# Kernel tuning notes

Measured on AMD Instinct MI355X. Metric: run time of the kernel, lower is better.

The kernel has to match this reference:

```python
import jax, jax.numpy as jnp
import numpy as np

IMG = 800          # original image H = W
OUT = 7            # pooled output size
SR = 2             # sampling_ratio
CANON_S = 224.0    # canonical_scale
CANON_L = 4.0      # canonical_level
EPS = 1e-6
KMIN, KMAX = 2, 5  # -log2 of first/last scale


def _bilinear_gather(feat, b_idx, y, x):
    """feat: [B,C,H,W]; b_idx: [N] int; y,x: [N,S] float sample coords.
    Returns [N,S,C]. Faithful to torchvision roi_align bilinear_interpolate
    (aligned=False semantics)."""
    B, C, H, W = feat.shape
    valid = (y > -1.0) & (y < H) & (x > -1.0) & (x < W)
    y = jnp.clip(y, 0.0, None)
    x = jnp.clip(x, 0.0, None)
    yl = jnp.minimum(jnp.floor(y).astype(jnp.int32), H - 1)
    xl = jnp.minimum(jnp.floor(x).astype(jnp.int32), W - 1)
    yh = jnp.minimum(yl + 1, H - 1)
    xh = jnp.minimum(xl + 1, W - 1)
    y = jnp.where(yl >= H - 1, yl.astype(y.dtype), y)
    x = jnp.where(xl >= W - 1, xl.astype(x.dtype), x)
    ly = y - yl
    lx = x - xl
    hy = 1.0 - ly
    hx = 1.0 - lx
    flat = feat.transpose(0, 2, 3, 1).reshape(B * H * W, C)  # [B*H*W, C]
    base = b_idx[:, None] * (H * W)                            # [N,1]

    def g(yy, xx):
        return flat[base + yy * W + xx]  # gather -> [N,S,C]

    val = ((hy * hx)[..., None] * g(yl, xl)
           + (hy * lx)[..., None] * g(yl, xh)
           + (ly * hx)[..., None] * g(yh, xl)
           + (ly * lx)[..., None] * g(yh, xh))
    return jnp.where(valid[..., None], val, 0.0)


def _roi_align(feat, rois, scale):
    """Single-level RoIAlign, aligned=False. rois: [N,5] = (batch_idx,x1,y1,x2,y2)."""
    N = rois.shape[0]
    C = feat.shape[1]
    b_idx = rois[:, 0].astype(jnp.int32)
    x1 = rois[:, 1] * scale
    y1 = rois[:, 2] * scale
    x2 = rois[:, 3] * scale
    y2 = rois[:, 4] * scale
    roi_w = jnp.maximum(x2 - x1, 1.0)
    roi_h = jnp.maximum(y2 - y1, 1.0)
    bin_w = roi_w / OUT
    bin_h = roi_h / OUT
    # sample offsets within the roi, in units of bins: [OUT*SR]
    off = (jnp.arange(OUT, dtype=feat.dtype)[:, None]
           + (jnp.arange(SR, dtype=feat.dtype)[None, :] + 0.5) / SR).reshape(-1)
    ys = y1[:, None] + off[None, :] * bin_h[:, None]  # [N, OUT*SR]
    xs = x1[:, None] + off[None, :] * bin_w[:, None]  # [N, OUT*SR]
    S = OUT * SR
    Y = jnp.broadcast_to(ys[:, :, None], (N, S, S)).reshape(N, S * S)
    X = jnp.broadcast_to(xs[:, None, :], (N, S, S)).reshape(N, S * S)
    val = _bilinear_gather(feat, b_idx, Y, X)          # [N, S*S, C]
    val = val.reshape(N, OUT, SR, OUT, SR, C).mean(axis=(2, 4))  # avg over samples
    return val.transpose(0, 3, 1, 2)                   # [N, C, OUT, OUT]


def setup_inputs() -> dict:
    key = jax.random.key(0)
    ks = jax.random.split(key, 7)
    feats = {}
    for i, hw in enumerate([200, 100, 50, 25]):
        feats[f"feat{i}"] = jax.random.normal(ks[i], (2, 256, hw, hw), dtype=jnp.float32)
    # boxes [2, 256, 4] in (x1,y1,x2,y2), sizes log-uniform in [16, ~590] px
    xy1 = jax.random.uniform(ks[4], (2, 256, 2), minval=0.0, maxval=IMG - 32.0)
    sz = 2.0 ** jax.random.uniform(ks[5], (2, 256, 2), minval=4.0, maxval=9.2)
    xy2 = jnp.minimum(xy1 + sz, float(IMG))
    boxes = jnp.concatenate([xy1, xy2], axis=-1).astype(jnp.float32)
    return {**feats, "boxes": boxes}


def reference(feat0, feat1, feat2, feat3, boxes):
    feats = [feat0, feat1, feat2, feat3]
    # _infer_scale: round(log2(feat_size / image_size)) -> power-of-two scale
    scales = [2.0 ** round(float(np.log2(f.shape[2] / IMG))) for f in feats]
    # _convert_to_roi_format
    B, Nb, _ = boxes.shape
    ids = jnp.repeat(jnp.arange(B, dtype=boxes.dtype), Nb)[:, None]
    rois = jnp.concatenate([ids, boxes.reshape(B * Nb, 4)], axis=1)  # [N,5]
    # LevelMapper (FPN eq.1)
    s = jnp.sqrt((rois[:, 3] - rois[:, 1]) * (rois[:, 4] - rois[:, 2]))
    lvls = jnp.floor(CANON_L + jnp.log2(s / CANON_S) + EPS)
    lvls = jnp.clip(lvls, KMIN, KMAX).astype(jnp.int32) - KMIN  # [N] in {0..3}
    out = jnp.zeros((B * Nb, feat0.shape[1], OUT, OUT), dtype=feat0.dtype)
    for lvl, (f, sc) in enumerate(zip(feats, scales)):
        r = _roi_align(f, rois, sc)
        out = jnp.where((lvls == lvl)[:, None, None, None], r, out)
    return out
```

## Files before the change

### kernel.cpp

```cpp
#include <hip/hip_runtime.h>
#include <hip/hip_bf16.h>


#define IMGC   256
#define OUTP   7
#define NBIN   49
#define SAMP   14
#define BT     128
#define TILE_LD (BT + 1)

#define WS_O1 20480000
#define WS_O2 25600000
#define WS_O3 26880000
#define WS_TOT 27200000

__global__ __launch_bounds__(256) void transpose_cl_kernel(
    const float* __restrict__ f0, const float* __restrict__ f1,
    const float* __restrict__ f2, const float* __restrict__ f3,
    float* __restrict__ ws)
{
    __shared__ float t[64][65];

    int bx = blockIdx.x;
    int lvl, r;
    if (bx < 5000)      { lvl = 0; r = bx; }
    else if (bx < 6256) { lvl = 1; r = bx - 5000; }
    else if (bx < 6576) { lvl = 2; r = bx - 6256; }
    else                { lvl = 3; r = bx - 6576; }

    const int  Mtab[4]  = {40000, 10000, 2500, 625};
    const int  Mttab[4] = {625, 157, 40, 10};
    const int  wsoff[4] = {0, WS_O1, WS_O2, WS_O3};

    const float* in = (lvl == 0) ? f0 : (lvl == 1) ? f1 : (lvl == 2) ? f2 : f3;
    float* outp = ws + wsoff[lvl];
    int M = Mtab[lvl];
    int Mt = Mttab[lvl];

    int mt   = r % Mt;
    int rest = r / Mt;
    int ct   = rest & 3;
    int bb   = rest >> 2;

    int tx = threadIdx.x & 63;
    int tg = threadIdx.x >> 6;
    int m0 = mt * 64;

    {
        int m = m0 + tx;
        if (m < M) {
            int base = (bb * IMGC + ct * 64) * M + m;
            #pragma unroll
            for (int k = 0; k < 16; ++k) {
                int cc = tg * 16 + k;
                t[cc][tx] = in[base + cc * M];
            }
        }
    }
    __syncthreads();
    #pragma unroll
    for (int k = 0; k < 16; ++k) {
        int mm = tg * 16 + k;
        int m = m0 + mm;
        if (m < M)
            outp[(bb * M + m) * IMGC + ct * 64 + tx] = t[tx][mm];
    }
}

template <bool CL>
__global__ __launch_bounds__(BT) void roialign_kernel(
    const float* __restrict__ f0, const float* __restrict__ f1,
    const float* __restrict__ f2, const float* __restrict__ f3,
    const float* __restrict__ boxes, float* __restrict__ out)
{
    __shared__ float s_ly[SAMP], s_wy[SAMP], s_lx[SAMP], s_wx[SAMP];
    __shared__ int   s_yol[SAMP], s_yoh[SAMP], s_xol[SAMP], s_xoh[SAMP];
    __shared__ float tile[NBIN * TILE_LD];

    const int tid = threadIdx.x;
    const int blk = blockIdx.x;
    const int n   = blk >> 1;
    const int c0  = (blk & 1) * BT;
    const int b   = n >> 8;

    const float x1 = boxes[n * 4 + 0];
    const float y1 = boxes[n * 4 + 1];
    const float x2 = boxes[n * 4 + 2];
    const float y2 = boxes[n * 4 + 3];

    float s = sqrtf(fmaxf((x2 - x1) * (y2 - y1), 1e-12f));
    float lf = floorf(4.0f + log2f(s / 224.0f) + 1e-6f);
    int lvl = (int)fminf(fmaxf(lf, 2.0f), 5.0f) - 2;

    const int   Htab[4]  = {200, 100, 50, 25};
    const float sctab[4] = {0.25f, 0.125f, 0.0625f, 0.03125f};
    const int   H = Htab[lvl];
    const int   W = H;
    const float scale = sctab[lvl];
    const float* fp = (lvl == 0) ? f0 : (lvl == 1) ? f1 : (lvl == 2) ? f2 : f3;

    const float x1s = x1 * scale, y1s = y1 * scale;
    const float x2s = x2 * scale, y2s = y2 * scale;
    const float roi_w = fmaxf(x2s - x1s, 1.0f);
    const float roi_h = fmaxf(y2s - y1s, 1.0f);
    const float bin_w = roi_w * (1.0f / OUTP);
    const float bin_h = roi_h * (1.0f / OUTP);

    if (tid < SAMP) {
        int t = tid;
        float off = (float)(t >> 1) + 0.25f + 0.5f * (float)(t & 1);
        float y = y1s + off * bin_h;
        float v = (y > -1.0f && y < (float)H) ? 1.0f : 0.0f;
        y = fmaxf(y, 0.0f);
        int yl = min((int)y, H - 1);
        int yh = min(yl + 1, H - 1);
        if (yl >= H - 1) y = (float)yl;
        s_ly[t] = y - (float)yl;
        s_wy[t] = v;
        if (CL) { s_yol[t] = ((b * H + yl) * W) * IMGC; s_yoh[t] = ((b * H + yh) * W) * IMGC; }
        else    { s_yol[t] = yl * W;                    s_yoh[t] = yh * W; }
    } else if (tid >= 64 && tid < 64 + SAMP) {
        int t = tid - 64;
        float off = (float)(t >> 1) + 0.25f + 0.5f * (float)(t & 1);
        float x = x1s + off * bin_w;
        float v = (x > -1.0f && x < (float)W) ? 1.0f : 0.0f;
        x = fmaxf(x, 0.0f);
        int xl = min((int)x, W - 1);
        int xh = min(xl + 1, W - 1);
        if (xl >= W - 1) x = (float)xl;
        s_lx[t] = x - (float)xl;
        s_wx[t] = v;
        if (CL) { s_xol[t] = xl * IMGC; s_xoh[t] = xh * IMGC; }
        else    { s_xol[t] = xl;        s_xoh[t] = xh; }
    }
    __syncthreads();

    const int c = c0 + tid;
    const int tb = CL ? c : (b * IMGC + c) * (H * W);

    for (int bin = 0; bin < NBIN; ++bin) {
        int ph = bin / OUTP;
        int pw = bin - ph * OUTP;
        float acc = 0.0f;
        #pragma unroll
        for (int sy = 0; sy < 2; ++sy) {
            #pragma unroll
            for (int sx = 0; sx < 2; ++sx) {
                int i = 2 * ph + sy;
                int j = 2 * pw + sx;
                float ly = s_ly[i], lx = s_lx[j];
                float hy = 1.0f - ly, hx = 1.0f - lx;
                float wm = s_wy[i] * s_wx[j];
                int yol = s_yol[i], yoh = s_yoh[i];
                int xol = s_xol[j], xoh = s_xoh[j];
                float v1 = fp[tb + yol + xol];
                float v2 = fp[tb + yol + xoh];
                float v3 = fp[tb + yoh + xol];
                float v4 = fp[tb + yoh + xoh];
                acc += wm * (hy * (hx * v1 + lx * v2) + ly * (hx * v3 + lx * v4));
            }
        }
        tile[bin * TILE_LD + tid] = acc * 0.25f;
    }
    __syncthreads();

    const int outbase = n * (IMGC * NBIN) + c0 * NBIN;
    for (int t = tid; t < BT * NBIN; t += BT) {
        int cl = t / NBIN;
        int bb = t - cl * NBIN;
        out[outbase + t] = tile[bb * TILE_LD + cl];
    }
}

extern "C" void kernel_launch(void* const* d_in, const int* in_sizes, int n_in,
                              void* d_out, int out_size, void* d_ws, size_t ws_size,
                              hipStream_t stream) {
    const float* f0    = (const float*)d_in[0];
    const float* f1    = (const float*)d_in[1];
    const float* f2    = (const float*)d_in[2];
    const float* f3    = (const float*)d_in[3];
    const float* boxes = (const float*)d_in[4];
    float* out = (float*)d_out;

    const bool use_cl = ws_size >= (size_t)WS_TOT * sizeof(float);

    if (use_cl) {
        float* w = (float*)d_ws;
        transpose_cl_kernel<<<6656, 256, 0, stream>>>(f0, f1, f2, f3, w);
        roialign_kernel<true><<<1024, BT, 0, stream>>>(
            w, w + WS_O1, w + WS_O2, w + WS_O3, boxes, out);
    } else {
        roialign_kernel<false><<<1024, BT, 0, stream>>>(f0, f1, f2, f3, boxes, out);
    }
}
```

Baseline: 202.2 us.

## Vectorize transpose and channels-last RoIAlign with float4 loads and precomputed weights

The transpose kernel gains a float4 path for full tiles, reading four spatial elements and writing four channels per thread through a padded shared tile. The channels-last RoIAlign kernel now has each thread handle four channels with float4 gathers, with work spread across bins by thread groups. It also precomputes the combined bilinear weights for all 14x14 sample pairs in shared memory. This cuts the number of memory instructions in the bandwidth-bound transpose and gather, at the cost of extra shared memory and a possible drop in occupancy.

```diff
diff --git a/kernel.cpp b/kernel.cpp
--- a/kernel.cpp
+++ b/kernel.cpp
@@ -7,7 +7,8 @@
 #define NBIN   49
 #define SAMP   14
 #define BT     128
-#define TILE_LD (BT + 1)
+#define TLD    132
+#define SLD    68
 
 #define WS_O1 20480000
 #define WS_O2 25600000
@@ -19,7 +20,7 @@
     const float* __restrict__ f2, const float* __restrict__ f3,
     float* __restrict__ ws)
 {
-    __shared__ float t[64][65];
+    __shared__ float t[64 * SLD];
 
     int bx = blockIdx.x;
     int lvl, r;
@@ -34,48 +35,75 @@
 
     const float* in = (lvl == 0) ? f0 : (lvl == 1) ? f1 : (lvl == 2) ? f2 : f3;
     float* outp = ws + wsoff[lvl];
-    int M = Mtab[lvl];
-    int Mt = Mttab[lvl];
+    const int M  = Mtab[lvl];
+    const int Mt = Mttab[lvl];
 
     int mt   = r % Mt;
     int rest = r / Mt;
     int ct   = rest & 3;
     int bb   = rest >> 2;
-
-    int tx = threadIdx.x & 63;
-    int tg = threadIdx.x >> 6;
-    int m0 = mt * 64;
-
-    {
-        int m = m0 + tx;
-        if (m < M) {
-            int base = (bb * IMGC + ct * 64) * M + m;
-            #pragma unroll
-            for (int k = 0; k < 16; ++k) {
-                int cc = tg * 16 + k;
-                t[cc][tx] = in[base + cc * M];
+    int m0   = mt * 64;
+
+    const bool vec = (m0 + 64 <= M) && ((M & 3) == 0);
+
+    if (vec) {
+        int mq = threadIdx.x & 15;
+        int cg = threadIdx.x >> 4;
+        const float* ibase = in + (bb * IMGC + ct * 64) * M + m0;
+        #pragma unroll
+        for (int j = 0; j < 4; ++j) {
+            int c = cg + 16 * j;
+            float4 v = *(const float4*)(ibase + c * M + 4 * mq);
+            *(float4*)&t[c * SLD + 4 * mq] = v;
+        }
+        __syncthreads();
+        int cq = threadIdx.x & 15;
+        int mr = threadIdx.x >> 4;
+        float* obase = outp + (bb * M + m0) * IMGC + ct * 64;
+        #pragma unroll
+        for (int j = 0; j < 4; ++j) {
+            int m = mr + 16 * j;
+            float4 v;
+            v.x = t[(4 * cq + 0) * SLD + m];
+            v.y = t[(4 * cq + 1) * SLD + m];
+            v.z = t[(4 * cq + 2) * SLD + m];
+            v.w = t[(4 * cq + 3) * SLD + m];
+            *(float4*)(obase + m * IMGC + 4 * cq) = v;
+        }
+    } else {
+        int tx = threadIdx.x & 63;
+        int tg = threadIdx.x >> 6;
+        {
+            int m = m0 + tx;
+            if (m < M) {
+                int base = (bb * IMGC + ct * 64) * M + m;
+                #pragma unroll
+                for (int k = 0; k < 16; ++k) {
+                    int cc = tg * 16 + k;
+                    t[cc * SLD + tx] = in[base + cc * M];
+                }
             }
         }
-    }
-    __syncthreads();
-    #pragma unroll
-    for (int k = 0; k < 16; ++k) {
-        int mm = tg * 16 + k;
-        int m = m0 + mm;
-        if (m < M)
-            outp[(bb * M + m) * IMGC + ct * 64 + tx] = t[tx][mm];
+        __syncthreads();
+        #pragma unroll
+        for (int k = 0; k < 16; ++k) {
+            int mm = tg * 16 + k;
+            int m = m0 + mm;
+            if (m < M)
+                outp[(bb * M + m) * IMGC + ct * 64 + tx] = t[tx * SLD + mm];
+        }
     }
 }
 
-template <bool CL>
-__global__ __launch_bounds__(BT) void roialign_kernel(
+__global__ __launch_bounds__(BT) void roialign_cl_kernel(
     const float* __restrict__ f0, const float* __restrict__ f1,
     const float* __restrict__ f2, const float* __restrict__ f3,
     const float* __restrict__ boxes, float* __restrict__ out)
 {
-    __shared__ float s_ly[SAMP], s_wy[SAMP], s_lx[SAMP], s_wx[SAMP];
-    __shared__ int   s_yol[SAMP], s_yoh[SAMP], s_xol[SAMP], s_xoh[SAMP];
-    __shared__ float tile[NBIN * TILE_LD];
+    __shared__ float  s_ly[SAMP], s_wy[SAMP], s_lx[SAMP], s_wx[SAMP];
+    __shared__ int    s_yol[SAMP], s_yoh[SAMP], s_xol[SAMP], s_xoh[SAMP];
+    __shared__ float4 s_w[SAMP * SAMP];
+    __shared__ float  tile[NBIN * TLD];
 
     const int tid = threadIdx.x;
     const int blk = blockIdx.x;
@@ -100,9 +128,8 @@
     const float* fp = (lvl == 0) ? f0 : (lvl == 1) ? f1 : (lvl == 2) ? f2 : f3;
 
     const float x1s = x1 * scale, y1s = y1 * scale;
-    const float x2s = x2 * scale, y2s = y2 * scale;
-    const float roi_w = fmaxf(x2s - x1s, 1.0f);
-    const float roi_h = fmaxf(y2s - y1s, 1.0f);
+    const float roi_w = fmaxf(x2 * scale - x1s, 1.0f);
+    const float roi_h = fmaxf(y2 * scale - y1s, 1.0f);
     const float bin_w = roi_w * (1.0f / OUTP);
     const float bin_h = roi_h * (1.0f / OUTP);
 
@@ -117,8 +144,8 @@
         if (yl >= H - 1) y = (float)yl;
         s_ly[t] = y - (float)yl;
         s_wy[t] = v;
-        if (CL) { s_yol[t] = ((b * H + yl) * W) * IMGC; s_yoh[t] = ((b * H + yh) * W) * IMGC; }
-        else    { s_yol[t] = yl * W;                    s_yoh[t] = yh * W; }
+        s_yol[t] = ((b * H + yl) * W) * (IMGC / 4);
+        s_yoh[t] = ((b * H + yh) * W) * (IMGC / 4);
     } else if (tid >= 64 && tid < 64 + SAMP) {
         int t = tid - 64;
         float off = (float)(t >> 1) + 0.25f + 0.5f * (float)(t & 1);
@@ -130,13 +157,131 @@
         if (xl >= W - 1) x = (float)xl;
         s_lx[t] = x - (float)xl;
         s_wx[t] = v;
-        if (CL) { s_xol[t] = xl * IMGC; s_xoh[t] = xh * IMGC; }
-        else    { s_xol[t] = xl;        s_xoh[t] = xh; }
-    }
-    __syncthreads();
-
-    const int c = c0 + tid;
-    const int tb = CL ? c : (b * IMGC + c) * (H * W);
+        s_xol[t] = xl * (IMGC / 4);
+        s_xoh[t] = xh * (IMGC / 4);
+    }
+    __syncthreads();
+
+    for (int idx = tid; idx < SAMP * SAMP; idx += BT) {
+        int i = idx / SAMP;
+        int j = idx - i * SAMP;
+        float v  = s_wy[i] * s_wx[j] * 0.25f;
+        float ly = s_ly[i], lx = s_lx[j];
+        float hy = 1.0f - ly, hx = 1.0f - lx;
+        float4 w;
+        w.x = v * hy * hx;
+        w.y = v * hy * lx;
+        w.z = v * ly * hx;
+        w.w = v * ly * lx;
+        s_w[idx] = w;
+    }
+    __syncthreads();
+
+    const int quad = tid & 31;
+    const int bg   = tid >> 5;
+    const float4* fp4 = (const float4*)fp + (c0 / 4) + quad;
+
+    for (int bin = bg; bin < NBIN; bin += 4) {
+        int ph = bin / OUTP;
+        int pw = bin - ph * OUTP;
+        float4 acc; acc.x = acc.y = acc.z = acc.w = 0.0f;
+        #pragma unroll
+        for (int sy = 0; sy < 2; ++sy) {
+            #pragma unroll
+            for (int sx = 0; sx < 2; ++sx) {
+                int i = 2 * ph + sy;
+                int j = 2 * pw + sx;
+                float4 w = s_w[i * SAMP + j];
+                int yol = s_yol[i], yoh = s_yoh[i];
+                int xol = s_xol[j], xoh = s_xoh[j];
+                float4 v1 = fp4[yol + xol];
+                float4 v2 = fp4[yol + xoh];
+                float4 v3 = fp4[yoh + xol];
+                float4 v4 = fp4[yoh + xoh];
+                acc.x += w.x * v1.x + w.y * v2.x + w.z * v3.x + w.w * v4.x;
+                acc.y += w.x * v1.y + w.y * v2.y + w.z * v3.y + w.w * v4.y;
+                acc.z += w.x * v1.z + w.y * v2.z + w.z * v3.z + w.w * v4.z;
+                acc.w += w.x * v1.w + w.y * v2.w + w.z * v3.w + w.w * v4.w;
+            }
+        }
+        *(float4*)&tile[bin * TLD + 4 * quad] = acc;
+    }
+    __syncthreads();
+
+    const int outbase = n * (IMGC * NBIN) + c0 * NBIN;
+    for (int t = tid; t < BT * NBIN; t += BT) {
+        int cl = t / NBIN;
+        int bb = t - cl * NBIN;
+        out[outbase + t] = tile[bb * TLD + cl];
+    }
+}
+
+__global__ __launch_bounds__(BT) void roialign_direct_kernel(
+    const float* __restrict__ f0, const float* __restrict__ f1,
+    const float* __restrict__ f2, const float* __restrict__ f3,
+    const float* __restrict__ boxes, float* __restrict__ out)
+{
+    __shared__ float s_ly[SAMP], s_wy[SAMP], s_lx[SAMP], s_wx[SAMP];
+    __shared__ int   s_yol[SAMP], s_yoh[SAMP], s_xol[SAMP], s_xoh[SAMP];
+    __shared__ float tile[NBIN * (BT + 1)];
+
+    const int tid = threadIdx.x;
+    const int blk = blockIdx.x;
+    const int n   = blk >> 1;
+    const int c0  = (blk & 1) * BT;
+    const int b   = n >> 8;
+
+    const float x1 = boxes[n * 4 + 0];
+    const float y1 = boxes[n * 4 + 1];
+    const float x2 = boxes[n * 4 + 2];
+    const float y2 = boxes[n * 4 + 3];
+
+    float s = sqrtf(fmaxf((x2 - x1) * (y2 - y1), 1e-12f));
+    float lf = floorf(4.0f + log2f(s / 224.0f) + 1e-6f);
+    int lvl = (int)fminf(fmaxf(lf, 2.0f), 5.0f) - 2;
+
+    const int   Htab[4]  = {200, 100, 50, 25};
+    const float sctab[4] = {0.25f, 0.125f, 0.0625f, 0.03125f};
+    const int   H = Htab[lvl];
+    const int   W = H;
+    const float scale = sctab[lvl];
+    const float* fp = (lvl == 0) ? f0 : (lvl == 1) ? f1 : (lvl == 2) ? f2 : f3;
+
+    const float x1s = x1 * scale, y1s = y1 * scale;
+    const float roi_w = fmaxf(x2 * scale - x1s, 1.0f);
+    const float roi_h = fmaxf(y2 * scale - y1s, 1.0f);
+    const float bin_w = roi_w * (1.0f / OUTP);
+    const float bin_h = roi_h * (1.0f / OUTP);
+
+    if (tid < SAMP) {
+        int t = tid;
+        float off = (float)(t >> 1) + 0.25f + 0.5f * (float)(t & 1);
+        float y = y1s + off * bin_h;
+        float v = (y > -1.0f && y < (float)H) ? 1.0f : 0.0f;
+        y = fmaxf(y, 0.0f);
+        int yl = min((int)y, H - 1);
+        int yh = min(yl + 1, H - 1);
+        if (yl >= H - 1) y = (float)yl;
+        s_ly[t] = y - (float)yl;
+        s_wy[t] = v;
+        s_yol[t] = yl * W; s_yoh[t] = yh * W;
+    } else if (tid >= 64 && tid < 64 + SAMP) {
+        int t = tid - 64;
+        float off = (float)(t >> 1) + 0.25f + 0.5f * (float)(t & 1);
+        float x = x1s + off * bin_w;
+        float v = (x > -1.0f && x < (float)W) ? 1.0f : 0.0f;
+        x = fmaxf(x, 0.0f);
+        int xl = min((int)x, W - 1);
+        int xh = min(xl + 1, W - 1);
+        if (xl >= W - 1) x = (float)xl;
+        s_lx[t] = x - (float)xl;
+        s_wx[t] = v;
+        s_xol[t] = xl; s_xoh[t] = xh;
+    }
+    __syncthreads();
+
+    const int c  = c0 + tid;
+    const int tb = (b * IMGC + c) * (H * W);
 
     for (int bin = 0; bin < NBIN; ++bin) {
         int ph = bin / OUTP;
@@ -151,16 +296,14 @@
                 float ly = s_ly[i], lx = s_lx[j];
                 float hy = 1.0f - ly, hx = 1.0f - lx;
                 float wm = s_wy[i] * s_wx[j];
-                int yol = s_yol[i], yoh = s_yoh[i];
-                int xol = s_xol[j], xoh = s_xoh[j];
-                float v1 = fp[tb + yol + xol];
-                float v2 = fp[tb + yol + xoh];
-                float v3 = fp[tb + yoh + xol];
-                float v4 = fp[tb + yoh + xoh];
+                float v1 = fp[tb + s_yol[i] + s_xol[j]];
+                float v2 = fp[tb + s_yol[i] + s_xoh[j]];
+                float v3 = fp[tb + s_yoh[i] + s_xol[j]];
+                float v4 = fp[tb + s_yoh[i] + s_xoh[j]];
                 acc += wm * (hy * (hx * v1 + lx * v2) + ly * (hx * v3 + lx * v4));
             }
         }
-        tile[bin * TILE_LD + tid] = acc * 0.25f;
+        tile[bin * (BT + 1) + tid] = acc * 0.25f;
     }
     __syncthreads();
 
@@ -168,7 +311,7 @@
     for (int t = tid; t < BT * NBIN; t += BT) {
         int cl = t / NBIN;
         int bb = t - cl * NBIN;
-        out[outbase + t] = tile[bb * TILE_LD + cl];
+        out[outbase + t] = tile[bb * (BT + 1) + cl];
     }
 }
 
@@ -187,9 +330,9 @@
     if (use_cl) {
         float* w = (float*)d_ws;
         transpose_cl_kernel<<<6656, 256, 0, stream>>>(f0, f1, f2, f3, w);
-        roialign_kernel<true><<<1024, BT, 0, stream>>>(
+        roialign_cl_kernel<<<1024, BT, 0, stream>>>(
             w, w + WS_O1, w + WS_O2, w + WS_O3, boxes, out);
     } else {
-        roialign_kernel<false><<<1024, BT, 0, stream>>>(f0, f1, f2, f3, boxes, out);
+        roialign_direct_kernel<<<1024, BT, 0, stream>>>(f0, f1, f2, f3, boxes, out);
     }
 }
```

Result: faster. 198.1 us (-2.0%).
